# Performance work log

Hardware: AMD Instinct MI355X
Metric: run time of the kernel (lower is better)

## Reference

```python
import jax, jax.numpy as jnp
import numpy as np

B, C, H, W = 8, 512, 32, 32
NUM_HEADS = 8
HEAD_DIM = C // NUM_HEADS


def setup_inputs() -> dict:
    key = jax.random.key(0)
    k1, k2, k3 = jax.random.split(key, 3)
    s = 0.02
    return {
        "x": jax.random.normal(k1, (B, C, H, W), dtype=jnp.float32),
        "W_qkv": jax.random.normal(k2, (3 * C, C), dtype=jnp.float32) * s,
        "b_qkv": jnp.zeros((3 * C,), dtype=jnp.float32),
        "W_proj": jax.random.normal(k3, (C, C), dtype=jnp.float32) * s,
        "b_proj": jnp.zeros((C,), dtype=jnp.float32),
    }


def reference(x, W_qkv, b_qkv, W_proj, b_proj):
    b, c, h, w = x.shape
    n = h * w  # seq_len in raster order
    nh, hd = NUM_HEADS, c // NUM_HEADS
    scale = hd ** -0.5

    # b c h w -> b n c
    x_seq = x.reshape(b, c, n).transpose(0, 2, 1)
    qkv = x_seq @ W_qkv.T + b_qkv  # (b, n, 3c)
    # b n (3 nh hd) -> 3, b, nh, n, hd
    qkv = qkv.reshape(b, n, 3, nh, hd).transpose(2, 0, 3, 1, 4)
    q, k, v = qkv[0], qkv[1], qkv[2]

    attn = jnp.einsum('bhnd,bhmd->bhnm', q, k) * scale
    causal = jnp.tril(jnp.ones((n, n), dtype=bool))
    attn = jnp.where(causal, attn, -jnp.inf)
    attn = jax.nn.softmax(attn, axis=-1)

    out = jnp.einsum('bhnm,bhmd->bhnd', attn, v)
    out = out.transpose(0, 2, 1, 3).reshape(b, n, c)  # b n c
    out = out @ W_proj.T + b_proj
    # b (h w) c -> b c h w
    return out.transpose(0, 2, 1).reshape(b, c, h, w)
```

## Files before the change

kernel.cpp:

```cpp
#include <hip/hip_runtime.h>
#include <hip/hip_bf16.h>
#include <math.h>

#define B_  8
#define C_  512
#define N_  1024
#define NH_ 8
#define HD_ 64
#define C3_ 1536

typedef __bf16 bf16x8  __attribute__((ext_vector_type(8)));
typedef __bf16 bf16x4v __attribute__((ext_vector_type(4)));
typedef float  f32x4   __attribute__((ext_vector_type(4)));
typedef __hip_bfloat16 bf16;

__device__ __forceinline__ f32x4 mfma16(const bf16x8& a, const bf16x8& b, const f32x4& c) {
    return __builtin_amdgcn_mfma_f32_16x16x32_bf16(a, b, c, 0, 0, 0);
}

__device__ __forceinline__ void ld_lds16(const bf16* g, bf16* l_uniform) {
    __builtin_amdgcn_global_load_lds(
        (const __attribute__((address_space(1))) void*)(uintptr_t)g,
        (__attribute__((address_space(3))) void*)(uintptr_t)l_uniform,
        16, 0, 0);
}

#define TRRD(d, a)    asm volatile("ds_read_b64_tr_b16 %0, %1"            : "=v"(d) : "v"(a))
#define TRRD128(d, a) asm volatile("ds_read_b64_tr_b16 %0, %1 offset:128" : "=v"(d) : "v"(a))


__global__ __launch_bounds__(256) void prep(const float* __restrict__ x,
                                            const float* __restrict__ Wq,
                                            const float* __restrict__ Wp,
                                            bf16* __restrict__ xb,
                                            bf16* __restrict__ Wqb,
                                            bf16* __restrict__ Wpb) {
    const int tid = threadIdx.x;
    if (blockIdx.x < 4096) {
        __shared__ float T[32][33];
        int t = blockIdx.x;
        const int n0 = (t & 31) * 32; t >>= 5;
        const int c0 = (t & 15) * 32; t >>= 4;
        const int b  = t;
        const int tx = tid & 31, ty = tid >> 5;
        const float* xp = x + ((size_t)b * C_ + c0) * N_ + n0;
#pragma unroll
        for (int l = 0; l < 4; ++l)
            T[ty + 8 * l][tx] = xp[(ty + 8 * l) * N_ + tx];
        __syncthreads();
        bf16* xo = xb + ((size_t)b * N_ + n0) * C_ + c0;
#pragma unroll
        for (int l = 0; l < 4; ++l)
            xo[(ty + 8 * l) * C_ + tx] = __float2bfloat16(T[tx][ty + 8 * l]);
    } else {
        const int base = (blockIdx.x - 4096) * 1024 + tid * 4;
        const float* src;
        bf16* dst;
        int off;
        if (base < C3_ * C_) { src = Wq; dst = Wqb; off = base; }
        else                 { src = Wp; dst = Wpb; off = base - C3_ * C_; }
        f32x4 w = *(const f32x4*)(src + off);
        bf16x4v o;
#pragma unroll
        for (int i = 0; i < 4; ++i) o[i] = (__bf16)w[i];
        *(bf16x4v*)(dst + off) = o;
    }
}

__global__ __launch_bounds__(256) void qkv_mfma(const bf16* __restrict__ xb,
                                                const bf16* __restrict__ Wqb,
                                                const float* __restrict__ bq,
                                                bf16* __restrict__ Qb,
                                                bf16* __restrict__ Kb,
                                                bf16* __restrict__ Vt) {
    __shared__ bf16 As[2][128 * 32];
    __shared__ bf16 Bs[2][128 * 32];
    __shared__ bf16 Vl[4][16][20];
    const int tid = threadIdx.x, w = tid >> 6, lane = tid & 63;
    const int lo = lane & 15, hi = lane >> 4;
    const int j0 = blockIdx.x * 128;
    const int m0 = blockIdx.y * 128;
    const int b  = m0 >> 10;

    const int srow = w * 32 + (lane >> 2);
    const int ss   = (srow & 3) ^ ((srow >> 2) & 3);
    const int scol = (((lane & 3) ^ ss)) * 8;
    const int sl   = (lane & 3) ^ ((lane >> 2) & 3);
    const bf16* gA = xb  + (size_t)(m0 + srow) * C_ + scol;
    const bf16* gB = Wqb + (size_t)(j0 + srow) * C_ + scol;
    const int lws = (w * 32) * 32;

    f32x4 acc[4][4];
#pragma unroll
    for (int mt = 0; mt < 4; ++mt)
#pragma unroll
        for (int jt = 0; jt < 4; ++jt)
            acc[mt][jt] = (f32x4){0.f, 0.f, 0.f, 0.f};

    auto STAGE = [&](bf16* Ab, bf16* Bb, int k0) {
        ld_lds16(gA + k0, Ab + lws);
        ld_lds16(gA + (size_t)16 * C_ + k0, Ab + lws + 16 * 32);
        ld_lds16(gB + k0, Bb + lws);
        ld_lds16(gB + (size_t)16 * C_ + k0, Bb + lws + 16 * 32);
    };
    auto COMPUTE = [&](const bf16* Ab, const bf16* Bb) {
        bf16x8 af[4], bfr[4];
#pragma unroll
        for (int mt = 0; mt < 4; ++mt)
            af[mt] = *(const bf16x8*)(Ab + ((w & 1) * 64 + mt * 16 + lo) * 32 + (hi ^ sl) * 8);
#pragma unroll
        for (int jt = 0; jt < 4; ++jt)
            bfr[jt] = *(const bf16x8*)(Bb + ((w >> 1) * 64 + jt * 16 + lo) * 32 + (hi ^ sl) * 8);
#pragma unroll
        for (int mt = 0; mt < 4; ++mt)
#pragma unroll
            for (int jt = 0; jt < 4; ++jt)
                acc[mt][jt] = mfma16(af[mt], bfr[jt], acc[mt][jt]);
    };

    STAGE(As[0], Bs[0], 0);
#pragma unroll
    for (int k0 = 0; k0 < C_; k0 += 64) {
        __syncthreads();
        if (k0 + 32 < C_) STAGE(As[1], Bs[1], k0 + 32);
        COMPUTE(As[0], Bs[0]);
        __syncthreads();
        if (k0 + 64 < C_) STAGE(As[0], Bs[0], k0 + 64);
        COMPUTE(As[1], Bs[1]);
    }

    const int jb = (w >> 1) * 64;
    const int nbase = (m0 & 1023) + (w & 1) * 64;
#pragma unroll
    for (int jt = 0; jt < 4; ++jt) {
        const int j16 = j0 + jb + jt * 16;
        const float bias = bq[j16 + lo];
        if (j16 < 512) {
            const int h = j16 >> 6, d = (j16 & 63) + lo;
            bf16* qp = Qb + ((size_t)(b * NH_ + h) * N_) * HD_ + d;
#pragma unroll
            for (int mt = 0; mt < 4; ++mt)
#pragma unroll
                for (int r = 0; r < 4; ++r) {
                    int n = nbase + mt * 16 + hi * 4 + r;
                    qp[(size_t)n * HD_] = __float2bfloat16((acc[mt][jt][r] + bias) * 0.18033688f);
                }
        } else if (j16 < 1024) {
            const int jj = j16 - 512;
            const int h = jj >> 6, d = (jj & 63) + lo;
            bf16* kp = Kb + ((size_t)(b * NH_ + h) * N_) * HD_ + d;
#pragma unroll
            for (int mt = 0; mt < 4; ++mt)
#pragma unroll
                for (int r = 0; r < 4; ++r) {
                    int n = nbase + mt * 16 + hi * 4 + r;
                    kp[(size_t)n * HD_] = __float2bfloat16(acc[mt][jt][r] + bias);
                }
        } else {
            const int jj = j16 - 1024;
            const int h = jj >> 6, dbase = jj & 63;
            bf16* vp = Vt + ((size_t)(b * NH_ + h) * HD_ + dbase) * N_ + nbase;
#pragma unroll
            for (int mt = 0; mt < 4; ++mt) {
#pragma unroll
                for (int r = 0; r < 4; ++r)
                    Vl[w][hi * 4 + r][lo] = __float2bfloat16(acc[mt][jt][r] + bias);
#pragma unroll
                for (int r = 0; r < 4; ++r)
                    vp[(size_t)(hi * 4 + r) * N_ + mt * 16 + lo] = Vl[w][lo][hi * 4 + r];
            }
        }
    }
}

__global__ __launch_bounds__(256) void attn_mfma(const bf16* __restrict__ Qb,
                                                 const bf16* __restrict__ Kb,
                                                 const bf16* __restrict__ Vt,
                                                 bf16* __restrict__ ao) {
    __shared__ bf16 Ks0[2][64 * 32], Ks1[2][64 * 32];
    __shared__ bf16 Vs0[2][64 * 32], Vs1[2][64 * 32];
    __shared__ __align__(16) bf16 PT[4][2][64][16];

    const int tid  = threadIdx.x;
    const int wv   = tid >> 6;
    const int lane = tid & 63;
    const int lo   = lane & 15;
    const int hi   = lane >> 4;
    const int bh   = blockIdx.x & 63;
    const int blk  = blockIdx.x >> 6;
    const int pi   = blk * 4 + wv;
    const int qwA  = pi * 16;
    const int qwB  = (63 - pi) * 16;

    const bf16* Qh = Qb + (size_t)bh * N_ * HD_;
    const bf16* Kh = Kb + (size_t)bh * N_ * HD_;
    const bf16* Vh = Vt + (size_t)bh * HD_ * N_;

    const bf16x8 qA0 = *(const bf16x8*)(Qh + (qwA + lo) * HD_ + hi * 8);
    const bf16x8 qA1 = *(const bf16x8*)(Qh + (qwA + lo) * HD_ + 32 + hi * 8);
    const bf16x8 qB0 = *(const bf16x8*)(Qh + (qwB + lo) * HD_ + hi * 8);
    const bf16x8 qB1 = *(const bf16x8*)(Qh + (qwB + lo) * HD_ + 32 + hi * 8);

    const int srow = tid >> 2;
    const int ss   = (srow & 3) ^ ((srow >> 2) & 3);
    const int scol = ((tid & 3) ^ ss) * 8;
    const int sl   = (lane & 3) ^ ((lane >> 2) & 3);
    const bf16* gK = Kh + (size_t)srow * HD_ + scol;
    const bf16* gV = Vh + (size_t)srow * N_ + scol;
    const int lofs = wv * 512;

    const unsigned ptA = (unsigned)(uintptr_t)&PT[wv][0][0][0]
                         + hi * 256 + (lo >> 2) * 32 + (lo & 3) * 8;
    const unsigned ptB = ptA + 2048;

    f32x4 OA[4], OB[4];
    float LA[4], LB[4];
#pragma unroll
    for (int r = 0; r < 4; ++r) {
        OA[0][r] = OA[1][r] = OA[2][r] = OA[3][r] = 0.f;
        OB[0][r] = OB[1][r] = OB[2][r] = OB[3][r] = 0.f;
        LA[r] = 0.f; LB[r] = 0.f;
    }

    const int nkbA   = (qwA + 79) >> 6;
    const int nkbB   = (qwB + 79) >> 6;
    const int nkbBlk = ((63 - blk * 4) * 16 + 79) >> 6;

    {
        ld_lds16(gK,      Ks0[0] + lofs);
        ld_lds16(gK + 32, Ks1[0] + lofs);
        ld_lds16(gV,      Vs0[0] + lofs);
        ld_lds16(gV + 32, Vs1[0] + lofs);
    }

    for (int kb = 0; kb < nkbBlk; ++kb) {
        const int key0 = kb * 64;
        const int cur  = kb & 1;

        __syncthreads();

        if (kb + 1 < nkbBlk) {
            const size_t nk = (size_t)(key0 + 64);
            ld_lds16(gK + nk * HD_,      Ks0[cur ^ 1] + lofs);
            ld_lds16(gK + nk * HD_ + 32, Ks1[cur ^ 1] + lofs);
            ld_lds16(gV + nk,            Vs0[cur ^ 1] + lofs);
            ld_lds16(gV + nk + 32,       Vs1[cur ^ 1] + lofs);
        }

        if (kb < nkbB) {
            const bool doA = (kb < nkbA);

            bf16x8 kf[4][2], vf[4][2];
#pragma unroll
            for (int t = 0; t < 4; ++t) {
                kf[t][0] = *(const bf16x8*)(Ks0[cur] + (t * 16 + lo) * 32 + (hi ^ sl) * 8);
                kf[t][1] = *(const bf16x8*)(Ks1[cur] + (t * 16 + lo) * 32 + (hi ^ sl) * 8);
                vf[t][0] = *(const bf16x8*)(Vs0[cur] + (t * 16 + lo) * 32 + (hi ^ sl) * 8);
                vf[t][1] = *(const bf16x8*)(Vs1[cur] + (t * 16 + lo) * 32 + (hi ^ sl) * 8);
            }

            f32x4 SB[4], SA[4];
#pragma unroll
            for (int t = 0; t < 4; ++t) {
                SB[t] = (f32x4){0.f, 0.f, 0.f, 0.f};
                SB[t] = mfma16(qB0, kf[t][0], SB[t]);
                SB[t] = mfma16(qB1, kf[t][1], SB[t]);
            }
            if (doA) {
#pragma unroll
                for (int t = 0; t < 4; ++t) {
                    SA[t] = (f32x4){0.f, 0.f, 0.f, 0.f};
                    SA[t] = mfma16(qA0, kf[t][0], SA[t]);
                    SA[t] = mfma16(qA1, kf[t][1], SA[t]);
                }
            }

            if (key0 + 63 > qwB) {
#pragma unroll
                for (int t = 0; t < 4; ++t)
#pragma unroll
                    for (int r = 0; r < 4; ++r)
                        if (key0 + t * 16 + lo > qwB + hi * 4 + r) SB[t][r] = -1e30f;
            }
            if (doA && key0 + 63 > qwA) {
#pragma unroll
                for (int t = 0; t < 4; ++t)
#pragma unroll
                    for (int r = 0; r < 4; ++r)
                        if (key0 + t * 16 + lo > qwA + hi * 4 + r) SA[t][r] = -1e30f;
            }

            bf16x4v pk;
#pragma unroll
            for (int t = 0; t < 4; ++t) {
#pragma unroll
                for (int r = 0; r < 4; ++r) {
                    float p = exp2f(SB[t][r]);
                    LB[r] += p;
                    pk[r] = (__bf16)p;
                }
                *(bf16x4v*)&PT[wv][1][t * 16 + lo][hi * 4] = pk;
            }
            if (doA) {
#pragma unroll
                for (int t = 0; t < 4; ++t) {
#pragma unroll
                    for (int r = 0; r < 4; ++r) {
                        float p = exp2f(SA[t][r]);
                        LA[r] += p;
                        pk[r] = (__bf16)p;
                    }
                    *(bf16x4v*)&PT[wv][0][t * 16 + lo][hi * 4] = pk;
                }
            }
            asm volatile("s_waitcnt lgkmcnt(0)" ::: "memory");

            bf16x4v b00, b01, b10, b11, a00, a01, a10, a11;
            TRRD(b00, ptB);          TRRD128(b01, ptB);
            TRRD(b10, ptB + 1024);   TRRD128(b11, ptB + 1024);
            if (doA) {
                TRRD(a00, ptA);        TRRD128(a01, ptA);
                TRRD(a10, ptA + 1024); TRRD128(a11, ptA + 1024);
            }
            asm volatile("s_waitcnt lgkmcnt(0)" ::: "memory");
            __builtin_amdgcn_sched_barrier(0);

            const bf16x8 paB0 = __builtin_shufflevector(b00, b01, 0, 1, 2, 3, 4, 5, 6, 7);
            const bf16x8 paB1 = __builtin_shufflevector(b10, b11, 0, 1, 2, 3, 4, 5, 6, 7);
#pragma unroll
            for (int t = 0; t < 4; ++t) {
                OB[t] = mfma16(paB0, vf[t][0], OB[t]);
                OB[t] = mfma16(paB1, vf[t][1], OB[t]);
            }
            if (doA) {
                const bf16x8 paA0 = __builtin_shufflevector(a00, a01, 0, 1, 2, 3, 4, 5, 6, 7);
                const bf16x8 paA1 = __builtin_shufflevector(a10, a11, 0, 1, 2, 3, 4, 5, 6, 7);
#pragma unroll
                for (int t = 0; t < 4; ++t) {
                    OA[t] = mfma16(paA0, vf[t][0], OA[t]);
                    OA[t] = mfma16(paA1, vf[t][1], OA[t]);
                }
            }
        }
    }

    const int b = bh >> 3, h = bh & 7;
#pragma unroll
    for (int c = 0; c < 2; ++c) {
        const int qw = c ? qwB : qwA;
        f32x4* O = c ? OB : OA;
        float* Lp = c ? LB : LA;
        float rL[4];
#pragma unroll
        for (int r = 0; r < 4; ++r) {
            float Ls = Lp[r];
#pragma unroll
            for (int off = 1; off < 16; off <<= 1)
                Ls += __shfl_xor(Ls, off, 64);
            rL[r] = 1.f / Ls;
        }
#pragma unroll
        for (int t = 0; t < 4; ++t)
#pragma unroll
            for (int r = 0; r < 4; ++r) {
                int q = qw + hi * 4 + r;
                ao[((size_t)b * N_ + q) * C_ + h * HD_ + t * 16 + lo] =
                    __float2bfloat16(O[t][r] * rL[r]);
            }
    }
}

__global__ __launch_bounds__(256) void proj_mfma(const bf16* __restrict__ aob,
                                                 const bf16* __restrict__ Wpb,
                                                 const float* __restrict__ bp,
                                                 float* __restrict__ out) {
    __shared__ bf16 As[2][64 * 32];
    __shared__ bf16 Bs[2][128 * 32];
    const int tid = threadIdx.x, w = tid >> 6, lane = tid & 63;
    const int lo = lane & 15, hi = lane >> 4;
    const int j0 = blockIdx.x * 64;
    const int n0 = blockIdx.y * 128;
    const int b  = n0 >> 10;

    const int r4 = lane >> 2;
    const int ss = (r4 & 3) ^ ((r4 >> 2) & 3);
    const int c8 = ((lane & 3) ^ ss) * 8;
    const int sl = (lane & 3) ^ ((lane >> 2) & 3);
    const bf16* gA = Wpb + (size_t)(j0 + w * 16 + r4) * C_ + c8;
    const bf16* gB = aob + (size_t)(n0 + w * 32 + r4) * C_ + c8;
    const int lwsA = (w * 16) * 32;
    const int lwsB = (w * 32) * 32;

    f32x4 acc[2][4];
#pragma unroll
    for (int mt = 0; mt < 2; ++mt)
#pragma unroll
        for (int jt = 0; jt < 4; ++jt)
            acc[mt][jt] = (f32x4){0.f, 0.f, 0.f, 0.f};

    auto STAGE = [&](bf16* Ab, bf16* Bb, int k0) {
        ld_lds16(gA + k0, Ab + lwsA);
        ld_lds16(gB + k0, Bb + lwsB);
        ld_lds16(gB + (size_t)16 * C_ + k0, Bb + lwsB + 16 * 32);
    };
    auto COMPUTE = [&](const bf16* Ab, const bf16* Bb) {
        bf16x8 af[2], bfr[4];
#pragma unroll
        for (int mt = 0; mt < 2; ++mt)
            af[mt] = *(const bf16x8*)(Ab + ((w & 1) * 32 + mt * 16 + lo) * 32 + (hi ^ sl) * 8);
#pragma unroll
        for (int jt = 0; jt < 4; ++jt)
            bfr[jt] = *(const bf16x8*)(Bb + ((w >> 1) * 64 + jt * 16 + lo) * 32 + (hi ^ sl) * 8);
#pragma unroll
        for (int mt = 0; mt < 2; ++mt)
#pragma unroll
            for (int jt = 0; jt < 4; ++jt)
                acc[mt][jt] = mfma16(af[mt], bfr[jt], acc[mt][jt]);
    };

    STAGE(As[0], Bs[0], 0);
#pragma unroll
    for (int k0 = 0; k0 < C_; k0 += 64) {
        __syncthreads();
        if (k0 + 32 < C_) STAGE(As[1], Bs[1], k0 + 32);
        COMPUTE(As[0], Bs[0]);
        __syncthreads();
        if (k0 + 64 < C_) STAGE(As[0], Bs[0], k0 + 64);
        COMPUTE(As[1], Bs[1]);
    }

#pragma unroll
    for (int mt = 0; mt < 2; ++mt)
#pragma unroll
        for (int r = 0; r < 4; ++r) {
            const int j = j0 + (w & 1) * 32 + mt * 16 + hi * 4 + r;
            const float bias = bp[j];
            float* op = out + ((size_t)(b * C_ + j)) * N_ + (n0 & 1023) + (w >> 1) * 64 + lo;
#pragma unroll
            for (int jt = 0; jt < 4; ++jt)
                op[jt * 16] = acc[mt][jt][r] + bias;
        }
}

extern "C" void kernel_launch(void* const* d_in, const int* in_sizes, int n_in,
                              void* d_out, int out_size, void* d_ws, size_t ws_size,
                              hipStream_t stream) {
    const float* x  = (const float*)d_in[0];
    const float* Wq = (const float*)d_in[1];
    const float* bq = (const float*)d_in[2];
    const float* Wp = (const float*)d_in[3];
    const float* bp = (const float*)d_in[4];
    float* out = (float*)d_out;

    const size_t headElems = (size_t)B_ * NH_ * N_ * HD_;
    bf16* xb  = (bf16*)d_ws;
    bf16* Wqb = xb + (size_t)B_ * N_ * C_;
    bf16* Wpb = Wqb + (size_t)C3_ * C_;
    bf16* Qb  = Wpb + (size_t)C_ * C_;
    bf16* Kb  = Qb + headElems;
    bf16* Vt  = Kb + headElems;
    bf16* aob = Vt + headElems;

    prep<<<dim3(4096 + 1024), dim3(256), 0, stream>>>(x, Wq, Wp, xb, Wqb, Wpb);

    qkv_mfma<<<dim3(C3_ / 128, (B_ * N_) / 128), dim3(256), 0, stream>>>(xb, Wqb, bq, Qb, Kb, Vt);
    attn_mfma<<<dim3(8 * 64), dim3(256), 0, stream>>>(Qb, Kb, Vt, aob);
    proj_mfma<<<dim3(C_ / 64, (B_ * N_) / 128), dim3(256), 0, stream>>>(aob, Wpb, bp, out);
}
```

Before: 139.4 us.

## Give each attention wave one query tile and double the grid

Each wave now processes a single 16-row query tile instead of a paired front and back tile. Within a block, two waves take early tiles and two take mirrored late tiles, and the grid doubles to 1024 blocks. This lowers per-wave register and LDS use (the P scratch buffer is halved) and raises parallelism and occupancy. In exchange, K/V tiles are loaded into LDS by twice as many blocks, and waves in the same block still have unequal trip counts.

```diff
diff --git a/kernel.cpp b/kernel.cpp
--- a/kernel.cpp
+++ b/kernel.cpp
@@ -179,7 +179,7 @@
                                                  bf16* __restrict__ ao) {
     __shared__ bf16 Ks0[2][64 * 32], Ks1[2][64 * 32];
     __shared__ bf16 Vs0[2][64 * 32], Vs1[2][64 * 32];
-    __shared__ __align__(16) bf16 PT[4][2][64][16];
+    __shared__ __align__(16) bf16 PT[4][64][16];
 
     const int tid  = threadIdx.x;
     const int wv   = tid >> 6;
@@ -187,19 +187,16 @@
     const int lo   = lane & 15;
     const int hi   = lane >> 4;
     const int bh   = blockIdx.x & 63;
-    const int blk  = blockIdx.x >> 6;
-    const int pi   = blk * 4 + wv;
-    const int qwA  = pi * 16;
-    const int qwB  = (63 - pi) * 16;
+    const int j    = blockIdx.x >> 6;
+    const int qt   = (wv < 2) ? (2 * j + wv) : (63 - 2 * j - (wv & 1));
+    const int qw   = qt * 16;
 
     const bf16* Qh = Qb + (size_t)bh * N_ * HD_;
     const bf16* Kh = Kb + (size_t)bh * N_ * HD_;
     const bf16* Vh = Vt + (size_t)bh * HD_ * N_;
 
-    const bf16x8 qA0 = *(const bf16x8*)(Qh + (qwA + lo) * HD_ + hi * 8);
-    const bf16x8 qA1 = *(const bf16x8*)(Qh + (qwA + lo) * HD_ + 32 + hi * 8);
-    const bf16x8 qB0 = *(const bf16x8*)(Qh + (qwB + lo) * HD_ + hi * 8);
-    const bf16x8 qB1 = *(const bf16x8*)(Qh + (qwB + lo) * HD_ + 32 + hi * 8);
+    const bf16x8 q0 = *(const bf16x8*)(Qh + (qw + lo) * HD_ + hi * 8);
+    const bf16x8 q1 = *(const bf16x8*)(Qh + (qw + lo) * HD_ + 32 + hi * 8);
 
     const int srow = tid >> 2;
     const int ss   = (srow & 3) ^ ((srow >> 2) & 3);
@@ -209,22 +206,19 @@
     const bf16* gV = Vh + (size_t)srow * N_ + scol;
     const int lofs = wv * 512;
 
-    const unsigned ptA = (unsigned)(uintptr_t)&PT[wv][0][0][0]
+    const unsigned ptW = (unsigned)(uintptr_t)&PT[wv][0][0]
                          + hi * 256 + (lo >> 2) * 32 + (lo & 3) * 8;
-    const unsigned ptB = ptA + 2048;
-
-    f32x4 OA[4], OB[4];
-    float LA[4], LB[4];
+
+    f32x4 O[4];
+    float L[4];
 #pragma unroll
     for (int r = 0; r < 4; ++r) {
-        OA[0][r] = OA[1][r] = OA[2][r] = OA[3][r] = 0.f;
-        OB[0][r] = OB[1][r] = OB[2][r] = OB[3][r] = 0.f;
-        LA[r] = 0.f; LB[r] = 0.f;
-    }
-
-    const int nkbA   = (qwA + 79) >> 6;
-    const int nkbB   = (qwB + 79) >> 6;
-    const int nkbBlk = ((63 - blk * 4) * 16 + 79) >> 6;
+        O[0][r] = O[1][r] = O[2][r] = O[3][r] = 0.f;
+        L[r] = 0.f;
+    }
+
+    const int nkbW   = (qw + 79) >> 6;
+    const int nkbBlk = ((63 - 2 * j) * 16 + 79) >> 6;
 
     {
         ld_lds16(gK,      Ks0[0] + lofs);
@@ -247,9 +241,7 @@
             ld_lds16(gV + nk + 32,       Vs1[cur ^ 1] + lofs);
         }
 
-        if (kb < nkbB) {
-            const bool doA = (kb < nkbA);
-
+        if (kb < nkbW) {
             bf16x8 kf[4][2], vf[4][2];
 #pragma unroll
             for (int t = 0; t < 4; ++t) {
@@ -259,35 +251,20 @@
                 vf[t][1] = *(const bf16x8*)(Vs1[cur] + (t * 16 + lo) * 32 + (hi ^ sl) * 8);
             }
 
-            f32x4 SB[4], SA[4];
+            f32x4 S[4];
 #pragma unroll
             for (int t = 0; t < 4; ++t) {
-                SB[t] = (f32x4){0.f, 0.f, 0.f, 0.f};
-                SB[t] = mfma16(qB0, kf[t][0], SB[t]);
-                SB[t] = mfma16(qB1, kf[t][1], SB[t]);
-            }
-            if (doA) {
-#pragma unroll
-                for (int t = 0; t < 4; ++t) {
-                    SA[t] = (f32x4){0.f, 0.f, 0.f, 0.f};
-                    SA[t] = mfma16(qA0, kf[t][0], SA[t]);
-                    SA[t] = mfma16(qA1, kf[t][1], SA[t]);
-                }
-            }
-
-            if (key0 + 63 > qwB) {
+                S[t] = (f32x4){0.f, 0.f, 0.f, 0.f};
+                S[t] = mfma16(q0, kf[t][0], S[t]);
+                S[t] = mfma16(q1, kf[t][1], S[t]);
+            }
+
+            if (key0 + 63 > qw) {
 #pragma unroll
                 for (int t = 0; t < 4; ++t)
 #pragma unroll
                     for (int r = 0; r < 4; ++r)
-                        if (key0 + t * 16 + lo > qwB + hi * 4 + r) SB[t][r] = -1e30f;
-            }
-            if (doA && key0 + 63 > qwA) {
-#pragma unroll
-                for (int t = 0; t < 4; ++t)
-#pragma unroll
-                    for (int r = 0; r < 4; ++r)
-                        if (key0 + t * 16 + lo > qwA + hi * 4 + r) SA[t][r] = -1e30f;
+                        if (key0 + t * 16 + lo > qw + hi * 4 + r) S[t][r] = -1e30f;
             }
 
             bf16x4v pk;
@@ -295,79 +272,48 @@
             for (int t = 0; t < 4; ++t) {
 #pragma unroll
                 for (int r = 0; r < 4; ++r) {
-                    float p = exp2f(SB[t][r]);
-                    LB[r] += p;
+                    float p = exp2f(S[t][r]);
+                    L[r] += p;
                     pk[r] = (__bf16)p;
                 }
-                *(bf16x4v*)&PT[wv][1][t * 16 + lo][hi * 4] = pk;
-            }
-            if (doA) {
-#pragma unroll
-                for (int t = 0; t < 4; ++t) {
-#pragma unroll
-                    for (int r = 0; r < 4; ++r) {
-                        float p = exp2f(SA[t][r]);
-                        LA[r] += p;
-                        pk[r] = (__bf16)p;
-                    }
-                    *(bf16x4v*)&PT[wv][0][t * 16 + lo][hi * 4] = pk;
-                }
+                *(bf16x4v*)&PT[wv][t * 16 + lo][hi * 4] = pk;
             }
             asm volatile("s_waitcnt lgkmcnt(0)" ::: "memory");
 
-            bf16x4v b00, b01, b10, b11, a00, a01, a10, a11;
-            TRRD(b00, ptB);          TRRD128(b01, ptB);
-            TRRD(b10, ptB + 1024);   TRRD128(b11, ptB + 1024);
-            if (doA) {
-                TRRD(a00, ptA);        TRRD128(a01, ptA);
-                TRRD(a10, ptA + 1024); TRRD128(a11, ptA + 1024);
-            }
+            bf16x4v p00, p01, p10, p11;
+            TRRD(p00, ptW);          TRRD128(p01, ptW);
+            TRRD(p10, ptW + 1024);   TRRD128(p11, ptW + 1024);
             asm volatile("s_waitcnt lgkmcnt(0)" ::: "memory");
             __builtin_amdgcn_sched_barrier(0);
 
-            const bf16x8 paB0 = __builtin_shufflevector(b00, b01, 0, 1, 2, 3, 4, 5, 6, 7);
-            const bf16x8 paB1 = __builtin_shufflevector(b10, b11, 0, 1, 2, 3, 4, 5, 6, 7);
+            const bf16x8 pa0 = __builtin_shufflevector(p00, p01, 0, 1, 2, 3, 4, 5, 6, 7);
+            const bf16x8 pa1 = __builtin_shufflevector(p10, p11, 0, 1, 2, 3, 4, 5, 6, 7);
 #pragma unroll
             for (int t = 0; t < 4; ++t) {
-                OB[t] = mfma16(paB0, vf[t][0], OB[t]);
-                OB[t] = mfma16(paB1, vf[t][1], OB[t]);
-            }
-            if (doA) {
-                const bf16x8 paA0 = __builtin_shufflevector(a00, a01, 0, 1, 2, 3, 4, 5, 6, 7);
-                const bf16x8 paA1 = __builtin_shufflevector(a10, a11, 0, 1, 2, 3, 4, 5, 6, 7);
-#pragma unroll
-                for (int t = 0; t < 4; ++t) {
-                    OA[t] = mfma16(paA0, vf[t][0], OA[t]);
-                    OA[t] = mfma16(paA1, vf[t][1], OA[t]);
-                }
+                O[t] = mfma16(pa0, vf[t][0], O[t]);
+                O[t] = mfma16(pa1, vf[t][1], O[t]);
             }
         }
     }
 
     const int b = bh >> 3, h = bh & 7;
-#pragma unroll
-    for (int c = 0; c < 2; ++c) {
-        const int qw = c ? qwB : qwA;
-        f32x4* O = c ? OB : OA;
-        float* Lp = c ? LB : LA;
-        float rL[4];
+    float rL[4];
+#pragma unroll
+    for (int r = 0; r < 4; ++r) {
+        float Ls = L[r];
+#pragma unroll
+        for (int off = 1; off < 16; off <<= 1)
+            Ls += __shfl_xor(Ls, off, 64);
+        rL[r] = 1.f / Ls;
+    }
+#pragma unroll
+    for (int t = 0; t < 4; ++t)
 #pragma unroll
         for (int r = 0; r < 4; ++r) {
-            float Ls = Lp[r];
-#pragma unroll
-            for (int off = 1; off < 16; off <<= 1)
-                Ls += __shfl_xor(Ls, off, 64);
-            rL[r] = 1.f / Ls;
+            int q = qw + hi * 4 + r;
+            ao[((size_t)b * N_ + q) * C_ + h * HD_ + t * 16 + lo] =
+                __float2bfloat16(O[t][r] * rL[r]);
         }
-#pragma unroll
-        for (int t = 0; t < 4; ++t)
-#pragma unroll
-            for (int r = 0; r < 4; ++r) {
-                int q = qw + hi * 4 + r;
-                ao[((size_t)b * N_ + q) * C_ + h * HD_ + t * 16 + lo] =
-                    __float2bfloat16(O[t][r] * rL[r]);
-            }
-    }
 }
 
 __global__ __launch_bounds__(256) void proj_mfma(const bf16* __restrict__ aob,
@@ -464,6 +410,6 @@
     prep<<<dim3(4096 + 1024), dim3(256), 0, stream>>>(x, Wq, Wp, xb, Wqb, Wpb);
 
     qkv_mfma<<<dim3(C3_ / 128, (B_ * N_) / 128), dim3(256), 0, stream>>>(xb, Wqb, bq, Qb, Kb, Vt);
-    attn_mfma<<<dim3(8 * 64), dim3(256), 0, stream>>>(Qb, Kb, Vt, aob);
+    attn_mfma<<<dim3(16 * 64), dim3(256), 0, stream>>>(Qb, Kb, Vt, aob);
     proj_mfma<<<dim3(C_ / 64, (B_ * N_) / 128), dim3(256), 0, stream>>>(aob, Wpb, bp, out);
 }
```

Result: no change. 141.7 us (+1.7%).

## Compute transposed scores so P feeds PV MFMA directly from registers

Applied to the files above, without the earlier changes.

Swaps the operands of the QK^T MFMA so each lane holds score values laid out as the A operand of the PV product. P then stays in registers and feeds 16x16x16 bf16 MFMAs, which removes the LDS round trip through the PT buffer, the transpose reads and the wait barriers. V fragments are now read as 4-element chunks per d-tile, and the row-sum reduction changes to match the new layout. The trade is twice as many smaller MFMA instructions plus extra LDS reads for V.

```diff
diff --git a/kernel.cpp b/kernel.cpp
--- a/kernel.cpp
+++ b/kernel.cpp
@@ -12,10 +12,29 @@
 typedef __bf16 bf16x8  __attribute__((ext_vector_type(8)));
 typedef __bf16 bf16x4v __attribute__((ext_vector_type(4)));
 typedef float  f32x4   __attribute__((ext_vector_type(4)));
+typedef short  short4v __attribute__((ext_vector_type(4)));
 typedef __hip_bfloat16 bf16;
 
 __device__ __forceinline__ f32x4 mfma16(const bf16x8& a, const bf16x8& b, const f32x4& c) {
     return __builtin_amdgcn_mfma_f32_16x16x32_bf16(a, b, c, 0, 0, 0);
+}
+
+__device__ __forceinline__ f32x4 mfma16k16(const bf16x4v& a, const bf16x4v& b, const f32x4& c) {
+#if defined(__HIP_DEVICE_COMPILE__) && __has_builtin(__builtin_amdgcn_mfma_f32_16x16x16bf16_1k)
+    short4v as, bs;
+    __builtin_memcpy(&as, &a, 8);
+    __builtin_memcpy(&bs, &b, 8);
+    return __builtin_amdgcn_mfma_f32_16x16x16bf16_1k(as, bs, c, 0, 0, 0);
+#elif defined(__HIP_DEVICE_COMPILE__) && __has_builtin(__builtin_amdgcn_mfma_f32_16x16x16_bf16)
+    return __builtin_amdgcn_mfma_f32_16x16x16_bf16(a, b, c, 0, 0, 0);
+#elif defined(__HIP_DEVICE_COMPILE__)
+    f32x4 d;
+    asm volatile("v_mfma_f32_16x16x16_bf16 %0, %1, %2, %3"
+                 : "=v"(d) : "v"(a), "v"(b), "v"(c));
+    return d;
+#else
+    return c;
+#endif
 }
 
 __device__ __forceinline__ void ld_lds16(const bf16* g, bf16* l_uniform) {
@@ -24,9 +43,6 @@
         (__attribute__((address_space(3))) void*)(uintptr_t)l_uniform,
         16, 0, 0);
 }
-
-#define TRRD(d, a)    asm volatile("ds_read_b64_tr_b16 %0, %1"            : "=v"(d) : "v"(a))
-#define TRRD128(d, a) asm volatile("ds_read_b64_tr_b16 %0, %1 offset:128" : "=v"(d) : "v"(a))
 
 
 __global__ __launch_bounds__(256) void prep(const float* __restrict__ x,
@@ -179,7 +195,6 @@
                                                  bf16* __restrict__ ao) {
     __shared__ bf16 Ks0[2][64 * 32], Ks1[2][64 * 32];
     __shared__ bf16 Vs0[2][64 * 32], Vs1[2][64 * 32];
-    __shared__ __align__(16) bf16 PT[4][2][64][16];
 
     const int tid  = threadIdx.x;
     const int wv   = tid >> 6;
@@ -209,17 +224,12 @@
     const bf16* gV = Vh + (size_t)srow * N_ + scol;
     const int lofs = wv * 512;
 
-    const unsigned ptA = (unsigned)(uintptr_t)&PT[wv][0][0][0]
-                         + hi * 256 + (lo >> 2) * 32 + (lo & 3) * 8;
-    const unsigned ptB = ptA + 2048;
-
     f32x4 OA[4], OB[4];
-    float LA[4], LB[4];
+    float LA = 0.f, LB = 0.f;
 #pragma unroll
     for (int r = 0; r < 4; ++r) {
         OA[0][r] = OA[1][r] = OA[2][r] = OA[3][r] = 0.f;
         OB[0][r] = OB[1][r] = OB[2][r] = OB[3][r] = 0.f;
-        LA[r] = 0.f; LB[r] = 0.f;
     }
 
     const int nkbA   = (qwA + 79) >> 6;
@@ -250,56 +260,55 @@
         if (kb < nkbB) {
             const bool doA = (kb < nkbA);
 
-            bf16x8 kf[4][2], vf[4][2];
+            bf16x8 kf[4][2];
 #pragma unroll
             for (int t = 0; t < 4; ++t) {
                 kf[t][0] = *(const bf16x8*)(Ks0[cur] + (t * 16 + lo) * 32 + (hi ^ sl) * 8);
                 kf[t][1] = *(const bf16x8*)(Ks1[cur] + (t * 16 + lo) * 32 + (hi ^ sl) * 8);
-                vf[t][0] = *(const bf16x8*)(Vs0[cur] + (t * 16 + lo) * 32 + (hi ^ sl) * 8);
-                vf[t][1] = *(const bf16x8*)(Vs1[cur] + (t * 16 + lo) * 32 + (hi ^ sl) * 8);
             }
 
             f32x4 SB[4], SA[4];
 #pragma unroll
             for (int t = 0; t < 4; ++t) {
                 SB[t] = (f32x4){0.f, 0.f, 0.f, 0.f};
-                SB[t] = mfma16(qB0, kf[t][0], SB[t]);
-                SB[t] = mfma16(qB1, kf[t][1], SB[t]);
+                SB[t] = mfma16(kf[t][0], qB0, SB[t]);
+                SB[t] = mfma16(kf[t][1], qB1, SB[t]);
             }
             if (doA) {
 #pragma unroll
                 for (int t = 0; t < 4; ++t) {
                     SA[t] = (f32x4){0.f, 0.f, 0.f, 0.f};
-                    SA[t] = mfma16(qA0, kf[t][0], SA[t]);
-                    SA[t] = mfma16(qA1, kf[t][1], SA[t]);
+                    SA[t] = mfma16(kf[t][0], qA0, SA[t]);
+                    SA[t] = mfma16(kf[t][1], qA1, SA[t]);
                 }
             }
 
             if (key0 + 63 > qwB) {
+                const int baseB = qwB + lo - key0 - 4 * hi;
 #pragma unroll
                 for (int t = 0; t < 4; ++t)
 #pragma unroll
                     for (int r = 0; r < 4; ++r)
-                        if (key0 + t * 16 + lo > qwB + hi * 4 + r) SB[t][r] = -1e30f;
+                        if (16 * t + r > baseB) SB[t][r] = -1e30f;
             }
             if (doA && key0 + 63 > qwA) {
+                const int baseA = qwA + lo - key0 - 4 * hi;
 #pragma unroll
                 for (int t = 0; t < 4; ++t)
 #pragma unroll
                     for (int r = 0; r < 4; ++r)
-                        if (key0 + t * 16 + lo > qwA + hi * 4 + r) SA[t][r] = -1e30f;
-            }
-
-            bf16x4v pk;
+                        if (16 * t + r > baseA) SA[t][r] = -1e30f;
+            }
+
+            bf16x4v pafB[4], pafA[4];
 #pragma unroll
             for (int t = 0; t < 4; ++t) {
 #pragma unroll
                 for (int r = 0; r < 4; ++r) {
                     float p = exp2f(SB[t][r]);
-                    LB[r] += p;
-                    pk[r] = (__bf16)p;
-                }
-                *(bf16x4v*)&PT[wv][1][t * 16 + lo][hi * 4] = pk;
+                    LB += p;
+                    pafB[t][r] = (__bf16)p;
+                }
             }
             if (doA) {
 #pragma unroll
@@ -307,38 +316,29 @@
 #pragma unroll
                     for (int r = 0; r < 4; ++r) {
                         float p = exp2f(SA[t][r]);
-                        LA[r] += p;
-                        pk[r] = (__bf16)p;
+                        LA += p;
+                        pafA[t][r] = (__bf16)p;
                     }
-                    *(bf16x4v*)&PT[wv][0][t * 16 + lo][hi * 4] = pk;
-                }
-            }
-            asm volatile("s_waitcnt lgkmcnt(0)" ::: "memory");
-
-            bf16x4v b00, b01, b10, b11, a00, a01, a10, a11;
-            TRRD(b00, ptB);          TRRD128(b01, ptB);
-            TRRD(b10, ptB + 1024);   TRRD128(b11, ptB + 1024);
-            if (doA) {
-                TRRD(a00, ptA);        TRRD128(a01, ptA);
-                TRRD(a10, ptA + 1024); TRRD128(a11, ptA + 1024);
-            }
-            asm volatile("s_waitcnt lgkmcnt(0)" ::: "memory");
-            __builtin_amdgcn_sched_barrier(0);
-
-            const bf16x8 paB0 = __builtin_shufflevector(b00, b01, 0, 1, 2, 3, 4, 5, 6, 7);
-            const bf16x8 paB1 = __builtin_shufflevector(b10, b11, 0, 1, 2, 3, 4, 5, 6, 7);
-#pragma unroll
-            for (int t = 0; t < 4; ++t) {
-                OB[t] = mfma16(paB0, vf[t][0], OB[t]);
-                OB[t] = mfma16(paB1, vf[t][1], OB[t]);
-            }
-            if (doA) {
-                const bf16x8 paA0 = __builtin_shufflevector(a00, a01, 0, 1, 2, 3, 4, 5, 6, 7);
-                const bf16x8 paA1 = __builtin_shufflevector(a10, a11, 0, 1, 2, 3, 4, 5, 6, 7);
-#pragma unroll
-                for (int t = 0; t < 4; ++t) {
-                    OA[t] = mfma16(paA0, vf[t][0], OA[t]);
-                    OA[t] = mfma16(paA1, vf[t][1], OA[t]);
+                }
+            }
+
+#pragma unroll
+            for (int td = 0; td < 4; ++td) {
+                const int row = (16 * td + lo) * 32;
+                bf16x4v vb[4];
+#pragma unroll
+                for (int tk = 0; tk < 4; ++tk) {
+                    const bf16* half = (tk < 2) ? Vs0[cur] : Vs1[cur];
+                    const int chunk = (2 * (tk & 1) + (hi >> 1)) ^ sl;
+                    vb[tk] = *(const bf16x4v*)(half + row + chunk * 8 + (hi & 1) * 4);
+                }
+#pragma unroll
+                for (int tk = 0; tk < 4; ++tk)
+                    OB[td] = mfma16k16(pafB[tk], vb[tk], OB[td]);
+                if (doA) {
+#pragma unroll
+                    for (int tk = 0; tk < 4; ++tk)
+                        OA[td] = mfma16k16(pafA[tk], vb[tk], OA[td]);
                 }
             }
         }
@@ -349,23 +349,21 @@
     for (int c = 0; c < 2; ++c) {
         const int qw = c ? qwB : qwA;
         f32x4* O = c ? OB : OA;
-        float* Lp = c ? LB : LA;
-        float rL[4];
-#pragma unroll
-        for (int r = 0; r < 4; ++r) {
-            float Ls = Lp[r];
-#pragma unroll
-            for (int off = 1; off < 16; off <<= 1)
-                Ls += __shfl_xor(Ls, off, 64);
-            rL[r] = 1.f / Ls;
-        }
+        float Ls = c ? LB : LA;
+        Ls += __shfl_xor(Ls, 16, 64);
+        Ls += __shfl_xor(Ls, 32, 64);
+        const float rL = 1.f / Ls;
+        float rLq[4];
+#pragma unroll
+        for (int r = 0; r < 4; ++r)
+            rLq[r] = __shfl(rL, 4 * hi + r, 64);
 #pragma unroll
         for (int t = 0; t < 4; ++t)
 #pragma unroll
             for (int r = 0; r < 4; ++r) {
                 int q = qw + hi * 4 + r;
                 ao[((size_t)b * N_ + q) * C_ + h * HD_ + t * 16 + lo] =
-                    __float2bfloat16(O[t][r] * rL[r]);
+                    __float2bfloat16(O[t][r] * rLq[r]);
             }
     }
 }
```

Measured after the change: 139.4 us. No clear change (+0.0%).
